# Kernel tuning notes

Hardware: AMD Instinct MI355X
Metric: run time of the kernel (lower is better)

Reference implementation:

```python
import jax, jax.numpy as jnp
import numpy as np

N = 65536      # bs * n_graphs * 32 electrodes
E = 1048576    # edges (avg degree 16)
H = 128        # first_hc (out_channels of GatedGraphConv)
IN = 5         # input node features
G = 16         # n_graphs (conv1d in-channels)
ELEC = 32
BS = 128
NC = 3


def setup_inputs() -> dict:
    key = jax.random.key(0)
    ks = jax.random.split(key, 14)
    s = 1.0 / np.sqrt(H)
    x = jax.random.normal(ks[0], (N, IN), dtype=jnp.float32)
    edge_index = jax.random.randint(ks[1], (2, E), 0, N, dtype=jnp.int32)
    edge_attr = jax.random.uniform(ks[2], (E,), dtype=jnp.float32)
    gconv_w = jax.random.normal(ks[3], (2, H, H), dtype=jnp.float32) * s
    gru_w_ih = jax.random.normal(ks[4], (3 * H, H), dtype=jnp.float32) * s
    gru_w_hh = jax.random.normal(ks[5], (3 * H, H), dtype=jnp.float32) * s
    gru_b_ih = jax.random.normal(ks[6], (3 * H,), dtype=jnp.float32) * s
    gru_b_hh = jax.random.normal(ks[7], (3 * H,), dtype=jnp.float32) * s
    conv_w = jax.random.normal(ks[8], (1, G, 3), dtype=jnp.float32) * (1.0 / np.sqrt(G * 3))
    conv_b = jax.random.normal(ks[9], (1,), dtype=jnp.float32) * 0.1
    L = (H - 3) // 2 + 1  # 63
    lin1_w = jax.random.normal(ks[10], (H, ELEC * L), dtype=jnp.float32) * (1.0 / np.sqrt(ELEC * L))
    lin1_b = jnp.zeros((H,), dtype=jnp.float32)
    lin2_w = jax.random.normal(ks[11], (NC, H), dtype=jnp.float32) * s
    lin2_b = jnp.zeros((NC,), dtype=jnp.float32)
    return {"x": x, "edge_index": edge_index, "edge_attr": edge_attr, "bs": BS,
            "gconv_w": gconv_w, "gru_w_ih": gru_w_ih, "gru_w_hh": gru_w_hh,
            "gru_b_ih": gru_b_ih, "gru_b_hh": gru_b_hh,
            "conv_w": conv_w, "conv_b": conv_b,
            "lin1_w": lin1_w, "lin1_b": lin1_b, "lin2_w": lin2_w, "lin2_b": lin2_b}


def _gated_graph_conv(x, edge_index, edge_attr, gconv_w, w_ih, w_hh, b_ih, b_hh):
    n = x.shape[0]
    # pad input features up to H (PyG GatedGraphConv behavior when in < out)
    h = jnp.concatenate([x, jnp.zeros((n, H - x.shape[1]), dtype=x.dtype)], axis=1)
    src, dst = edge_index[0], edge_index[1]
    for i in range(2):  # num_layers = 2
        m = h @ gconv_w[i]                              # [N, H]
        msg = m[src] * edge_attr[:, None]               # gather + edge weight
        agg = jax.ops.segment_sum(msg, dst, num_segments=n)  # scatter-add
        # GRUCell(agg, h)
        gi = agg @ w_ih.T + b_ih
        gh = h @ w_hh.T + b_hh
        i_r, i_z, i_n = jnp.split(gi, 3, axis=1)
        h_r, h_z, h_n = jnp.split(gh, 3, axis=1)
        r = jax.nn.sigmoid(i_r + h_r)
        z = jax.nn.sigmoid(i_z + h_z)
        nn_ = jnp.tanh(i_n + r * h_n)
        h = (1.0 - z) * nn_ + z * h
    return h


def reference(x, edge_index, edge_attr, bs, gconv_w, gru_w_ih, gru_w_hh,
              gru_b_ih, gru_b_hh, conv_w, conv_b, lin1_w, lin1_b, lin2_w, lin2_b):
    h = _gated_graph_conv(x, edge_index, edge_attr, gconv_w,
                          gru_w_ih, gru_w_hh, gru_b_ih, gru_b_hh)
    h = jax.nn.relu(h)  # dropout is identity in eval mode
    g = h.shape[0] // (bs * ELEC)
    # (bs g e) f -> (bs e) g f
    h = h.reshape(bs, g, ELEC, H).transpose(0, 2, 1, 3).reshape(bs * ELEC, g, H)
    h = jax.lax.conv_general_dilated(h, conv_w, window_strides=(2,), padding='VALID',
                                     dimension_numbers=('NCH', 'OIH', 'NCH'))
    h = h + conv_b[None, :, None]
    h = jax.nn.relu(h[:, 0, :])                 # squeeze channel -> [bs*e, L]
    h = h.reshape(bs, -1)                       # (bs e) f -> bs (e f)
    h = jax.nn.relu(h @ lin1_w.T + lin1_b)
    h = h @ lin2_w.T + lin2_b
    return jax.nn.softmax(h, axis=-1)
```

## Files before the change

kernel.cpp:

```cpp
#include <hip/hip_runtime.h>
#include <math.h>

#define NN 65536
#define NE 1048576
#define HH 128
#define ELEC 32
#define BSZ 128
#define NB 512

typedef unsigned short ushort_t;
typedef __bf16 bf16x8 __attribute__((ext_vector_type(8)));
typedef float f32x16 __attribute__((ext_vector_type(16)));

#define MFMA(A, B, C) __builtin_amdgcn_mfma_f32_32x32x16_bf16(A, B, C, 0, 0, 0)

__device__ __forceinline__ float sigm(float x) { return 1.f / (1.f + __expf(-x)); }
__device__ __forceinline__ float tanh_fast(float x) { return 2.f / (1.f + __expf(-2.f * x)) - 1.f; }

__device__ __forceinline__ float bf2f(ushort_t u) {
    union { unsigned int i; float f; } v; v.i = ((unsigned int)u) << 16; return v.f;
}
__device__ __forceinline__ ushort_t f2bf(float f) {
    union { float f; unsigned int i; } v; v.f = f;
    unsigned int r = (v.i + 0x7fffu + ((v.i >> 16) & 1u)) >> 16;
    return (ushort_t)r;
}


__global__ void k_init(const float* __restrict__ x, ushort_t* __restrict__ xh) {
    int i = blockIdx.x * 256 + threadIdx.x;
    int n = i >> 7, c = i & 127;
    float v = (c < 5) ? x[n * 5 + c] : 0.f;
    xh[(size_t)n * 256 + 128 + c] = f2bf(v);
}

__global__ __launch_bounds__(256) void k_bhist(const int* __restrict__ dst,
                                               int* __restrict__ bcnt) {
    __shared__ int h[NB];
    int t = threadIdx.x;
    h[t] = 0; h[t + 256] = 0;
    __syncthreads();
    int e0 = blockIdx.x * 4096;
    #pragma unroll
    for (int i = 0; i < 16; ++i)
        atomicAdd(&h[dst[e0 + i * 256 + t] >> 7], 1);
    __syncthreads();
    int c0 = h[t];       if (c0) atomicAdd(&bcnt[t], c0);
    int c1 = h[t + 256]; if (c1) atomicAdd(&bcnt[t + 256], c1);
}

__global__ void k_bscan(const int* __restrict__ bcnt, int* __restrict__ boffs,
                        int* __restrict__ bcur) {
    __shared__ int s[NB];
    int t = threadIdx.x;
    int v = bcnt[t];
    s[t] = v;
    __syncthreads();
    for (int d = 1; d < NB; d <<= 1) {
        int u = (t >= d) ? s[t - d] : 0;
        __syncthreads();
        s[t] += u;
        __syncthreads();
    }
    int ex = s[t] - v;
    boffs[t] = ex;
    bcur[t] = ex;
    if (t == NB - 1) boffs[NB] = s[t];
}

__global__ __launch_bounds__(256) void k_bpart(const int* __restrict__ src,
        const int* __restrict__ dst, const float* __restrict__ ea,
        int* __restrict__ bcur, uint2* __restrict__ ebkt) {
    __shared__ int lcnt[NB];
    __shared__ int base[NB];
    __shared__ int lcur[NB];
    int t = threadIdx.x;
    lcnt[t] = 0; lcnt[t + 256] = 0;
    lcur[t] = 0; lcur[t + 256] = 0;
    __syncthreads();
    int e0 = blockIdx.x * 4096;
    #pragma unroll
    for (int i = 0; i < 16; ++i)
        atomicAdd(&lcnt[dst[e0 + i * 256 + t] >> 7], 1);
    __syncthreads();
    {
        int c = lcnt[t];
        base[t] = c ? atomicAdd(&bcur[t], c) : 0;
        c = lcnt[t + 256];
        base[t + 256] = c ? atomicAdd(&bcur[t + 256], c) : 0;
    }
    __syncthreads();
    #pragma unroll
    for (int i = 0; i < 16; ++i) {
        int e = e0 + i * 256 + t;
        int d = dst[e];
        int bk = d >> 7;
        int pos = base[bk] + atomicAdd(&lcur[bk], 1);
        uint2 pk;
        pk.x = (unsigned int)src[e] | ((unsigned int)(d & 127) << 16);
        pk.y = __float_as_uint(ea[e]);
        ebkt[pos] = pk;
    }
}

__global__ __launch_bounds__(256) void k_csc(const int* __restrict__ boffs,
        const uint2* __restrict__ ebkt, uint2* __restrict__ epack,
        int* __restrict__ offs) {
    __shared__ int cnt[128];
    __shared__ int s[128];
    __shared__ int base[128];
    int b = blockIdx.x, t = threadIdx.x;
    if (t < 128) cnt[t] = 0;
    __syncthreads();
    int e0 = boffs[b], e1 = boffs[b + 1];
    for (int i = e0 + t; i < e1; i += 256)
        atomicAdd(&cnt[(ebkt[i].x >> 16) & 127], 1);
    __syncthreads();
    if (t < 128) s[t] = cnt[t];
    __syncthreads();
    for (int d = 1; d < 128; d <<= 1) {
        int v = (t < 128 && t >= d) ? s[t - d] : 0;
        __syncthreads();
        if (t < 128) s[t] += v;
        __syncthreads();
    }
    if (t < 128) {
        int bs = e0 + s[t] - cnt[t];
        base[t] = bs;
        offs[b * 128 + t] = bs;
        cnt[t] = 0;
    }
    if (b == 0 && t == 255) offs[NN] = NE;
    __syncthreads();
    for (int i = e0 + t; i < e1; i += 256) {
        uint2 e = ebkt[i];
        int dl = (e.x >> 16) & 127;
        int pos = base[dl] + atomicAdd(&cnt[dl], 1);
        epack[pos] = e;
    }
}

__global__ void k_prep(const float* __restrict__ wih, const float* __restrict__ whh,
                       const float* __restrict__ gw,
                       ushort_t* __restrict__ vp, ushort_t* __restrict__ gp) {
    int b = blockIdx.x, t = threadIdx.x;
    if (b < 512) {
        int i = b * 256 + t;
        int rho = i >> 8, k = i & 255;
        int q = rho >> 7, g = (rho >> 5) & 3, cc = rho & 31;
        int c = q * 32 + cc;
        float v;
        if (g == 0)      v = (k < 128) ? wih[c * 128 + k]          : whh[c * 128 + k - 128];
        else if (g == 1) v = (k < 128) ? wih[(128 + c) * 128 + k]  : whh[(128 + c) * 128 + k - 128];
        else if (g == 2) v = (k < 128) ? wih[(256 + c) * 128 + k]  : 0.f;
        else             v = (k < 128) ? 0.f                       : whh[(256 + c) * 128 + k - 128];
        int ks = k >> 4, lh = (k >> 3) & 1, j = k & 7, lr = cc;
        vp[(size_t)(ks * 16 + q * 4 + g) * 512 + (lh * 32 + lr) * 8 + j] = f2bf(v);
    } else {
        int i = (b - 512) * 256 + t;
        int l = i >> 14, r = i & 16383, c = r >> 7, k = r & 127;
        float v = gw[l * 16384 + k * 128 + c];
        int ct = c >> 5, lr = c & 31;
        int ks = k >> 4, lh = (k >> 3) & 1, j = k & 7;
        gp[(size_t)((l * 8 + ks) * 4 + ct) * 512 + (lh * 32 + lr) * 8 + j] = f2bf(v);
    }
}

__global__ __launch_bounds__(256, 2) void k_mgemm(const ushort_t* __restrict__ gp,
        const ushort_t* __restrict__ xh, ushort_t* __restrict__ m) {
    int t = threadIdx.x;
    int lane = t & 63, w = t >> 6;
    int lr = lane & 31, lh = lane >> 5;
    int n0 = blockIdx.x * 256 + w * 64;
    f32x16 acc[2][4];
    #pragma unroll
    for (int nt = 0; nt < 2; ++nt)
        #pragma unroll
        for (int ct = 0; ct < 4; ++ct)
            #pragma unroll
            for (int r = 0; r < 16; ++r) acc[nt][ct][r] = 0.f;
    size_t rowA0 = (size_t)(n0 + lr) * 256 + 128;
    size_t rowA1 = rowA0 + 32 * 256;
    #pragma unroll
    for (int ks = 0; ks < 8; ++ks) {
        int kg = ks * 16 + lh * 8;
        bf16x8 ah0 = *reinterpret_cast<const bf16x8*>(xh + rowA0 + kg);
        bf16x8 ah1 = *reinterpret_cast<const bf16x8*>(xh + rowA1 + kg);
        #pragma unroll
        for (int ct = 0; ct < 4; ++ct) {
            bf16x8 bh = *reinterpret_cast<const bf16x8*>(gp + (size_t)(ks * 4 + ct) * 512 + lane * 8);
            acc[0][ct] = MFMA(ah0, bh, acc[0][ct]);
            acc[1][ct] = MFMA(ah1, bh, acc[1][ct]);
        }
    }
    #pragma unroll
    for (int nt = 0; nt < 2; ++nt)
        #pragma unroll
        for (int ct = 0; ct < 4; ++ct)
            #pragma unroll
            for (int r = 0; r < 16; ++r) {
                int row = (r & 3) + 8 * (r >> 2) + 4 * lh;
                m[(size_t)(n0 + nt * 32 + row) * 128 + ct * 32 + lr] = f2bf(acc[nt][ct][r]);
            }
}

__global__ __launch_bounds__(256) void k_gather(const ushort_t* __restrict__ m,
        const int* __restrict__ offs, const uint2* __restrict__ epack,
        ushort_t* __restrict__ xh) {
    int n = blockIdx.x * 4 + (threadIdx.x >> 6);
    int lane = threadIdx.x & 63;
    int k0 = offs[n], k1 = offs[n + 1];
    float a0 = 0.f, a1 = 0.f;
    int k = k0;
    if (k < k1 && (k & 1)) {
        uint2 e = epack[k];
        float w = __uint_as_float(e.y);
        ushort2 u = *reinterpret_cast<const ushort2*>(m + (size_t)(e.x & 0xFFFFu) * HH + 2 * lane);
        a0 = fmaf(w, bf2f(u.x), a0);
        a1 = fmaf(w, bf2f(u.y), a1);
        ++k;
    }
    for (; k + 4 <= k1; k += 4) {
        uint4 e01 = *reinterpret_cast<const uint4*>(epack + k);
        uint4 e23 = *reinterpret_cast<const uint4*>(epack + k + 2);
        ushort2 u0 = *reinterpret_cast<const ushort2*>(m + (size_t)(e01.x & 0xFFFFu) * HH + 2 * lane);
        ushort2 u1 = *reinterpret_cast<const ushort2*>(m + (size_t)(e01.z & 0xFFFFu) * HH + 2 * lane);
        ushort2 u2 = *reinterpret_cast<const ushort2*>(m + (size_t)(e23.x & 0xFFFFu) * HH + 2 * lane);
        ushort2 u3 = *reinterpret_cast<const ushort2*>(m + (size_t)(e23.z & 0xFFFFu) * HH + 2 * lane);
        float w0 = __uint_as_float(e01.y), w1 = __uint_as_float(e01.w);
        float w2 = __uint_as_float(e23.y), w3 = __uint_as_float(e23.w);
        a0 = fmaf(w0, bf2f(u0.x), a0); a1 = fmaf(w0, bf2f(u0.y), a1);
        a0 = fmaf(w1, bf2f(u1.x), a0); a1 = fmaf(w1, bf2f(u1.y), a1);
        a0 = fmaf(w2, bf2f(u2.x), a0); a1 = fmaf(w2, bf2f(u2.y), a1);
        a0 = fmaf(w3, bf2f(u3.x), a0); a1 = fmaf(w3, bf2f(u3.y), a1);
    }
    if (k + 2 <= k1) {
        uint4 e01 = *reinterpret_cast<const uint4*>(epack + k);
        ushort2 u0 = *reinterpret_cast<const ushort2*>(m + (size_t)(e01.x & 0xFFFFu) * HH + 2 * lane);
        ushort2 u1 = *reinterpret_cast<const ushort2*>(m + (size_t)(e01.z & 0xFFFFu) * HH + 2 * lane);
        float w0 = __uint_as_float(e01.y), w1 = __uint_as_float(e01.w);
        a0 = fmaf(w0, bf2f(u0.x), a0); a1 = fmaf(w0, bf2f(u0.y), a1);
        a0 = fmaf(w1, bf2f(u1.x), a0); a1 = fmaf(w1, bf2f(u1.y), a1);
        k += 2;
    }
    if (k < k1) {
        uint2 e = epack[k];
        float w = __uint_as_float(e.y);
        ushort2 u = *reinterpret_cast<const ushort2*>(m + (size_t)(e.x & 0xFFFFu) * HH + 2 * lane);
        a0 = fmaf(w, bf2f(u.x), a0);
        a1 = fmaf(w, bf2f(u.y), a1);
    }
    ushort2 o; o.x = f2bf(a0); o.y = f2bf(a1);
    *reinterpret_cast<ushort2*>(xh + (size_t)n * 256 + 2 * lane) = o;
}

__global__ __launch_bounds__(256, 2) void k_gru(const ushort_t* __restrict__ vp,
        ushort_t* __restrict__ xh,
        const float* __restrict__ bih, const float* __restrict__ bhh) {
    int t = threadIdx.x;
    int lane = t & 63, q = t >> 6;
    int lr = lane & 31, lh = lane >> 5;
    int n0 = blockIdx.x * 64;
    f32x16 acc[2][4];
    #pragma unroll
    for (int nt = 0; nt < 2; ++nt)
        #pragma unroll
        for (int g = 0; g < 4; ++g)
            #pragma unroll
            for (int r = 0; r < 16; ++r) acc[nt][g][r] = 0.f;

    size_t rowA0 = (size_t)(n0 + lr) * 256;
    size_t rowA1 = rowA0 + 32 * 256;
    #pragma unroll
    for (int ks = 0; ks < 16; ++ks) {
        int kg = ks * 16 + lh * 8;
        bf16x8 ah0 = *reinterpret_cast<const bf16x8*>(xh + rowA0 + kg);
        bf16x8 ah1 = *reinterpret_cast<const bf16x8*>(xh + rowA1 + kg);
        #pragma unroll
        for (int g = 0; g < 4; ++g) {
            bf16x8 b = *reinterpret_cast<const bf16x8*>(vp + (size_t)(ks * 16 + q * 4 + g) * 512 + lane * 8);
            acc[0][g] = MFMA(ah0, b, acc[0][g]);
            acc[1][g] = MFMA(ah1, b, acc[1][g]);
        }
    }

    __syncthreads();

    int c = q * 32 + lr;
    float brz = bih[c] + bhh[c];
    float bzz = bih[128 + c] + bhh[128 + c];
    float bin = bih[256 + c];
    float bhn = bhh[256 + c];
    #pragma unroll
    for (int nt = 0; nt < 2; ++nt) {
        #pragma unroll
        for (int r = 0; r < 16; ++r) {
            int node = n0 + nt * 32 + (r & 3) + 8 * (r >> 2) + 4 * lh;
            float rg = sigm(acc[nt][0][r] + brz);
            float zg = sigm(acc[nt][1][r] + bzz);
            float nn = tanh_fast(acc[nt][2][r] + bin + rg * (acc[nt][3][r] + bhn));
            size_t idx = (size_t)node * 256 + 128 + c;
            float hold = bf2f(xh[idx]);
            float hnew = (1.f - zg) * nn + zg * hold;
            xh[idx] = f2bf(hnew);
        }
    }
}

__global__ __launch_bounds__(64) void k_conv(const ushort_t* __restrict__ xh,
        const float* __restrict__ cw, const float* __restrict__ cb,
        float* __restrict__ co) {
    __shared__ float tile[16 * 128];
    __shared__ float w[48];
    int be = blockIdx.x;
    int b = be >> 5, e = be & 31;
    int t = threadIdx.x;
    if (t < 48) w[t] = cw[t];
    #pragma unroll
    for (int i = 0; i < 8; ++i) {
        int f = t + i * 64;
        int g = f >> 5, c4 = f & 31;
        size_t idx = (size_t)(b * 512 + g * 32 + e) * 256 + 128 + c4 * 4;
        ushort4 vh4 = *reinterpret_cast<const ushort4*>(xh + idx);
        float* dst = tile + g * 128 + c4 * 4;
        dst[0] = fmaxf(bf2f(vh4.x), 0.f);
        dst[1] = fmaxf(bf2f(vh4.y), 0.f);
        dst[2] = fmaxf(bf2f(vh4.z), 0.f);
        dst[3] = fmaxf(bf2f(vh4.w), 0.f);
    }
    __syncthreads();
    if (t < 63) {
        float s = cb[0];
        #pragma unroll
        for (int g = 0; g < 16; ++g) {
            const float* p = tile + g * 128 + 2 * t;
            s = fmaf(p[0], w[g * 3 + 0], s);
            s = fmaf(p[1], w[g * 3 + 1], s);
            s = fmaf(p[2], w[g * 3 + 2], s);
        }
        co[b * 2016 + e * 63 + t] = fmaxf(s, 0.f);
    }
}

__global__ __launch_bounds__(128) void k_lin1(const float* __restrict__ co,
        const float* __restrict__ w, const float* __restrict__ bias,
        float* __restrict__ fc1) {
    __shared__ float v[2016];
    int b = blockIdx.x, t = threadIdx.x;
    for (int i = t; i < 2016; i += 128) v[i] = co[b * 2016 + i];
    __syncthreads();
    float s = bias[t];
    const float* wr = w + t * 2016;
    for (int k = 0; k < 2016; k += 4) {
        float4 wv = *reinterpret_cast<const float4*>(wr + k);
        s = fmaf(wv.x, v[k + 0], s);
        s = fmaf(wv.y, v[k + 1], s);
        s = fmaf(wv.z, v[k + 2], s);
        s = fmaf(wv.w, v[k + 3], s);
    }
    fc1[b * 128 + t] = fmaxf(s, 0.f);
}

__global__ __launch_bounds__(128) void k_lin2(const float* __restrict__ fc1,
        const float* __restrict__ w, const float* __restrict__ bias,
        float* __restrict__ out) {
    int b = threadIdx.x;
    float s0 = bias[0], s1 = bias[1], s2 = bias[2];
    const float* v = fc1 + b * 128;
    for (int k = 0; k < 128; ++k) {
        float x = v[k];
        s0 = fmaf(x, w[k], s0);
        s1 = fmaf(x, w[128 + k], s1);
        s2 = fmaf(x, w[256 + k], s2);
    }
    float mx = fmaxf(s0, fmaxf(s1, s2));
    float e0 = __expf(s0 - mx), e1 = __expf(s1 - mx), e2 = __expf(s2 - mx);
    float inv = 1.f / (e0 + e1 + e2);
    out[b * 3 + 0] = e0 * inv;
    out[b * 3 + 1] = e1 * inv;
    out[b * 3 + 2] = e2 * inv;
}

extern "C" void kernel_launch(void* const* d_in, const int* in_sizes, int n_in,
                              void* d_out, int out_size, void* d_ws, size_t ws_size,
                              hipStream_t stream) {
    const float* x   = (const float*)d_in[0];
    const int*   ei  = (const int*)d_in[1];
    const float* ea  = (const float*)d_in[2];
    const float* gw  = (const float*)d_in[4];
    const float* wih = (const float*)d_in[5];
    const float* whh = (const float*)d_in[6];
    const float* bih = (const float*)d_in[7];
    const float* bhh = (const float*)d_in[8];
    const float* cw  = (const float*)d_in[9];
    const float* cb  = (const float*)d_in[10];
    const float* l1w = (const float*)d_in[11];
    const float* l1b = (const float*)d_in[12];
    const float* l2w = (const float*)d_in[13];
    const float* l2b = (const float*)d_in[14];
    float* out = (float*)d_out;

    char* p = (char*)d_ws;
    ushort_t* xh  = (ushort_t*)p; p += (size_t)NN * 256 * 2;
    ushort_t* vp  = (ushort_t*)p; p += 512 * 256 * 2;
    ushort_t* gp  = (ushort_t*)p; p += 2 * 128 * 128 * 2;
    ushort_t* m   = (ushort_t*)p; p += (size_t)NN * HH * 2;
    uint2* ebkt   = (uint2*)p;   p += (size_t)NE * 8;
    uint2* epack  = (uint2*)p;   p += (size_t)NE * 8;
    float* co  = (float*)p; p += (size_t)BSZ * 2016 * 4;
    float* fc1 = (float*)p; p += (size_t)BSZ * HH * 4;
    int* bcnt  = (int*)p; p += NB * 4;
    int* boffs = (int*)p; p += (NB + 1) * 4;
    int* bcur  = (int*)p; p += NB * 4;
    int* offs  = (int*)p; p += (size_t)(NN + 1) * 4;

    const int* src = ei;
    const int* dst = ei + NE;

    k_prep<<<640, 256, 0, stream>>>(wih, whh, gw, vp, gp);
    hipMemsetAsync(bcnt, 0, NB * 4, stream);
    k_bhist<<<256, 256, 0, stream>>>(dst, bcnt);
    k_bscan<<<1, 512, 0, stream>>>(bcnt, boffs, bcur);
    k_bpart<<<256, 256, 0, stream>>>(src, dst, ea, bcur, ebkt);
    k_csc<<<NB, 256, 0, stream>>>(boffs, ebkt, epack, offs);
    k_init<<<(NN * 128) / 256, 256, 0, stream>>>(x, xh);

    for (int layer = 0; layer < 2; ++layer) {
        k_mgemm<<<NN / 256, 256, 0, stream>>>(gp + (size_t)layer * 16384, xh, m);
        k_gather<<<NN / 4, 256, 0, stream>>>(m, offs, epack, xh);
        k_gru<<<NN / 64, 256, 0, stream>>>(vp, xh, bih, bhh);
    }

    k_conv<<<BSZ * ELEC, 64, 0, stream>>>(xh, cw, cb, co);
    k_lin1<<<BSZ, 128, 0, stream>>>(co, l1w, l1b, fc1);
    k_lin2<<<1, 128, 0, stream>>>(fc1, l2w, l2b, out);
}
```

Before: 401.5 us.

## Fuse edge aggregation into GRU kernel via swizzled LDS staging

Merges the separate gather and GRU kernels into one kernel. Each block first aggregates messages for its 64 nodes into a bank-swizzled shared-memory tile, then runs the GRU MFMA with the aggregated half read from LDS. The hidden state buffer shrinks from a 256-wide concatenated layout to 128 wide. This removes the aggregate round trip through global memory and one launch per layer. In exchange, each wave walks 16 nodes serially during the gather phase, which lowers gather parallelism and latency hiding, and the 16KB LDS tile may affect occupancy.

```diff
diff --git a/kernel.cpp b/kernel.cpp
--- a/kernel.cpp
+++ b/kernel.cpp
@@ -27,26 +27,26 @@
 }
 
 
-__global__ void k_init(const float* __restrict__ x, ushort_t* __restrict__ xh) {
+__global__ void k_init(const float* __restrict__ x, ushort_t* __restrict__ h) {
     int i = blockIdx.x * 256 + threadIdx.x;
     int n = i >> 7, c = i & 127;
     float v = (c < 5) ? x[n * 5 + c] : 0.f;
-    xh[(size_t)n * 256 + 128 + c] = f2bf(v);
+    h[(size_t)n * 128 + c] = f2bf(v);
 }
 
 __global__ __launch_bounds__(256) void k_bhist(const int* __restrict__ dst,
                                                int* __restrict__ bcnt) {
-    __shared__ int h[NB];
-    int t = threadIdx.x;
-    h[t] = 0; h[t + 256] = 0;
+    __shared__ int hh[NB];
+    int t = threadIdx.x;
+    hh[t] = 0; hh[t + 256] = 0;
     __syncthreads();
     int e0 = blockIdx.x * 4096;
     #pragma unroll
     for (int i = 0; i < 16; ++i)
-        atomicAdd(&h[dst[e0 + i * 256 + t] >> 7], 1);
-    __syncthreads();
-    int c0 = h[t];       if (c0) atomicAdd(&bcnt[t], c0);
-    int c1 = h[t + 256]; if (c1) atomicAdd(&bcnt[t + 256], c1);
+        atomicAdd(&hh[dst[e0 + i * 256 + t] >> 7], 1);
+    __syncthreads();
+    int c0 = hh[t];       if (c0) atomicAdd(&bcnt[t], c0);
+    int c1 = hh[t + 256]; if (c1) atomicAdd(&bcnt[t + 256], c1);
 }
 
 __global__ void k_bscan(const int* __restrict__ bcnt, int* __restrict__ boffs,
@@ -167,7 +167,7 @@
 }
 
 __global__ __launch_bounds__(256, 2) void k_mgemm(const ushort_t* __restrict__ gp,
-        const ushort_t* __restrict__ xh, ushort_t* __restrict__ m) {
+        const ushort_t* __restrict__ h, ushort_t* __restrict__ m) {
     int t = threadIdx.x;
     int lane = t & 63, w = t >> 6;
     int lr = lane & 31, lh = lane >> 5;
@@ -179,13 +179,13 @@
         for (int ct = 0; ct < 4; ++ct)
             #pragma unroll
             for (int r = 0; r < 16; ++r) acc[nt][ct][r] = 0.f;
-    size_t rowA0 = (size_t)(n0 + lr) * 256 + 128;
-    size_t rowA1 = rowA0 + 32 * 256;
+    size_t rowA0 = (size_t)(n0 + lr) * 128;
+    size_t rowA1 = rowA0 + 32 * 128;
     #pragma unroll
     for (int ks = 0; ks < 8; ++ks) {
         int kg = ks * 16 + lh * 8;
-        bf16x8 ah0 = *reinterpret_cast<const bf16x8*>(xh + rowA0 + kg);
-        bf16x8 ah1 = *reinterpret_cast<const bf16x8*>(xh + rowA1 + kg);
+        bf16x8 ah0 = *reinterpret_cast<const bf16x8*>(h + rowA0 + kg);
+        bf16x8 ah1 = *reinterpret_cast<const bf16x8*>(h + rowA1 + kg);
         #pragma unroll
         for (int ct = 0; ct < 4; ++ct) {
             bf16x8 bh = *reinterpret_cast<const bf16x8*>(gp + (size_t)(ks * 4 + ct) * 512 + lane * 8);
@@ -204,63 +204,79 @@
             }
 }
 
-__global__ __launch_bounds__(256) void k_gather(const ushort_t* __restrict__ m,
+__global__ __launch_bounds__(256, 2) void k_aggru(const ushort_t* __restrict__ m,
         const int* __restrict__ offs, const uint2* __restrict__ epack,
-        ushort_t* __restrict__ xh) {
-    int n = blockIdx.x * 4 + (threadIdx.x >> 6);
-    int lane = threadIdx.x & 63;
-    int k0 = offs[n], k1 = offs[n + 1];
-    float a0 = 0.f, a1 = 0.f;
-    int k = k0;
-    if (k < k1 && (k & 1)) {
-        uint2 e = epack[k];
-        float w = __uint_as_float(e.y);
-        ushort2 u = *reinterpret_cast<const ushort2*>(m + (size_t)(e.x & 0xFFFFu) * HH + 2 * lane);
-        a0 = fmaf(w, bf2f(u.x), a0);
-        a1 = fmaf(w, bf2f(u.y), a1);
-        ++k;
-    }
-    for (; k + 4 <= k1; k += 4) {
-        uint4 e01 = *reinterpret_cast<const uint4*>(epack + k);
-        uint4 e23 = *reinterpret_cast<const uint4*>(epack + k + 2);
-        ushort2 u0 = *reinterpret_cast<const ushort2*>(m + (size_t)(e01.x & 0xFFFFu) * HH + 2 * lane);
-        ushort2 u1 = *reinterpret_cast<const ushort2*>(m + (size_t)(e01.z & 0xFFFFu) * HH + 2 * lane);
-        ushort2 u2 = *reinterpret_cast<const ushort2*>(m + (size_t)(e23.x & 0xFFFFu) * HH + 2 * lane);
-        ushort2 u3 = *reinterpret_cast<const ushort2*>(m + (size_t)(e23.z & 0xFFFFu) * HH + 2 * lane);
-        float w0 = __uint_as_float(e01.y), w1 = __uint_as_float(e01.w);
-        float w2 = __uint_as_float(e23.y), w3 = __uint_as_float(e23.w);
-        a0 = fmaf(w0, bf2f(u0.x), a0); a1 = fmaf(w0, bf2f(u0.y), a1);
-        a0 = fmaf(w1, bf2f(u1.x), a0); a1 = fmaf(w1, bf2f(u1.y), a1);
-        a0 = fmaf(w2, bf2f(u2.x), a0); a1 = fmaf(w2, bf2f(u2.y), a1);
-        a0 = fmaf(w3, bf2f(u3.x), a0); a1 = fmaf(w3, bf2f(u3.y), a1);
-    }
-    if (k + 2 <= k1) {
-        uint4 e01 = *reinterpret_cast<const uint4*>(epack + k);
-        ushort2 u0 = *reinterpret_cast<const ushort2*>(m + (size_t)(e01.x & 0xFFFFu) * HH + 2 * lane);
-        ushort2 u1 = *reinterpret_cast<const ushort2*>(m + (size_t)(e01.z & 0xFFFFu) * HH + 2 * lane);
-        float w0 = __uint_as_float(e01.y), w1 = __uint_as_float(e01.w);
-        a0 = fmaf(w0, bf2f(u0.x), a0); a1 = fmaf(w0, bf2f(u0.y), a1);
-        a0 = fmaf(w1, bf2f(u1.x), a0); a1 = fmaf(w1, bf2f(u1.y), a1);
-        k += 2;
-    }
-    if (k < k1) {
-        uint2 e = epack[k];
-        float w = __uint_as_float(e.y);
-        ushort2 u = *reinterpret_cast<const ushort2*>(m + (size_t)(e.x & 0xFFFFu) * HH + 2 * lane);
-        a0 = fmaf(w, bf2f(u.x), a0);
-        a1 = fmaf(w, bf2f(u.y), a1);
-    }
-    ushort2 o; o.x = f2bf(a0); o.y = f2bf(a1);
-    *reinterpret_cast<ushort2*>(xh + (size_t)n * 256 + 2 * lane) = o;
-}
-
-__global__ __launch_bounds__(256, 2) void k_gru(const ushort_t* __restrict__ vp,
-        ushort_t* __restrict__ xh,
+        const ushort_t* __restrict__ vp, ushort_t* __restrict__ h,
         const float* __restrict__ bih, const float* __restrict__ bhh) {
+    __shared__ ushort_t aggl[64 * 128];
     int t = threadIdx.x;
     int lane = t & 63, q = t >> 6;
+    int n0 = blockIdx.x * 64;
+
+    {
+        int chunk = lane >> 2;
+        int woff = (lane & 3) * 2;
+        for (int nl = q * 16; nl < q * 16 + 16; ++nl) {
+            int n = n0 + nl;
+            int k0 = offs[n], k1 = offs[n + 1];
+            float a0 = 0.f, a1 = 0.f;
+            int k = k0;
+            for (; k + 8 <= k1; k += 8) {
+                uint4 ea_ = *reinterpret_cast<const uint4*>(epack + k);
+                uint4 eb_ = *reinterpret_cast<const uint4*>(epack + k + 2);
+                uint4 ec_ = *reinterpret_cast<const uint4*>(epack + k + 4);
+                uint4 ed_ = *reinterpret_cast<const uint4*>(epack + k + 6);
+                ushort2 u0 = *reinterpret_cast<const ushort2*>(m + (size_t)(ea_.x & 0xFFFFu) * HH + 2 * lane);
+                ushort2 u1 = *reinterpret_cast<const ushort2*>(m + (size_t)(ea_.z & 0xFFFFu) * HH + 2 * lane);
+                ushort2 u2 = *reinterpret_cast<const ushort2*>(m + (size_t)(eb_.x & 0xFFFFu) * HH + 2 * lane);
+                ushort2 u3 = *reinterpret_cast<const ushort2*>(m + (size_t)(eb_.z & 0xFFFFu) * HH + 2 * lane);
+                ushort2 u4 = *reinterpret_cast<const ushort2*>(m + (size_t)(ec_.x & 0xFFFFu) * HH + 2 * lane);
+                ushort2 u5 = *reinterpret_cast<const ushort2*>(m + (size_t)(ec_.z & 0xFFFFu) * HH + 2 * lane);
+                ushort2 u6 = *reinterpret_cast<const ushort2*>(m + (size_t)(ed_.x & 0xFFFFu) * HH + 2 * lane);
+                ushort2 u7 = *reinterpret_cast<const ushort2*>(m + (size_t)(ed_.z & 0xFFFFu) * HH + 2 * lane);
+                float w0 = __uint_as_float(ea_.y), w1 = __uint_as_float(ea_.w);
+                float w2 = __uint_as_float(eb_.y), w3 = __uint_as_float(eb_.w);
+                float w4 = __uint_as_float(ec_.y), w5 = __uint_as_float(ec_.w);
+                float w6 = __uint_as_float(ed_.y), w7 = __uint_as_float(ed_.w);
+                a0 = fmaf(w0, bf2f(u0.x), a0); a1 = fmaf(w0, bf2f(u0.y), a1);
+                a0 = fmaf(w1, bf2f(u1.x), a0); a1 = fmaf(w1, bf2f(u1.y), a1);
+                a0 = fmaf(w2, bf2f(u2.x), a0); a1 = fmaf(w2, bf2f(u2.y), a1);
+                a0 = fmaf(w3, bf2f(u3.x), a0); a1 = fmaf(w3, bf2f(u3.y), a1);
+                a0 = fmaf(w4, bf2f(u4.x), a0); a1 = fmaf(w4, bf2f(u4.y), a1);
+                a0 = fmaf(w5, bf2f(u5.x), a0); a1 = fmaf(w5, bf2f(u5.y), a1);
+                a0 = fmaf(w6, bf2f(u6.x), a0); a1 = fmaf(w6, bf2f(u6.y), a1);
+                a0 = fmaf(w7, bf2f(u7.x), a0); a1 = fmaf(w7, bf2f(u7.y), a1);
+            }
+            if (k + 4 <= k1) {
+                uint4 ea_ = *reinterpret_cast<const uint4*>(epack + k);
+                uint4 eb_ = *reinterpret_cast<const uint4*>(epack + k + 2);
+                ushort2 u0 = *reinterpret_cast<const ushort2*>(m + (size_t)(ea_.x & 0xFFFFu) * HH + 2 * lane);
+                ushort2 u1 = *reinterpret_cast<const ushort2*>(m + (size_t)(ea_.z & 0xFFFFu) * HH + 2 * lane);
+                ushort2 u2 = *reinterpret_cast<const ushort2*>(m + (size_t)(eb_.x & 0xFFFFu) * HH + 2 * lane);
+                ushort2 u3 = *reinterpret_cast<const ushort2*>(m + (size_t)(eb_.z & 0xFFFFu) * HH + 2 * lane);
+                float w0 = __uint_as_float(ea_.y), w1 = __uint_as_float(ea_.w);
+                float w2 = __uint_as_float(eb_.y), w3 = __uint_as_float(eb_.w);
+                a0 = fmaf(w0, bf2f(u0.x), a0); a1 = fmaf(w0, bf2f(u0.y), a1);
+                a0 = fmaf(w1, bf2f(u1.x), a0); a1 = fmaf(w1, bf2f(u1.y), a1);
+                a0 = fmaf(w2, bf2f(u2.x), a0); a1 = fmaf(w2, bf2f(u2.y), a1);
+                a0 = fmaf(w3, bf2f(u3.x), a0); a1 = fmaf(w3, bf2f(u3.y), a1);
+                k += 4;
+            }
+            for (; k < k1; ++k) {
+                uint2 e = epack[k];
+                float w = __uint_as_float(e.y);
+                ushort2 u = *reinterpret_cast<const ushort2*>(m + (size_t)(e.x & 0xFFFFu) * HH + 2 * lane);
+                a0 = fmaf(w, bf2f(u.x), a0);
+                a1 = fmaf(w, bf2f(u.y), a1);
+            }
+            ushort2 o; o.x = f2bf(a0); o.y = f2bf(a1);
+            int sw = chunk ^ (nl & 15);
+            *reinterpret_cast<ushort2*>(aggl + nl * 128 + sw * 8 + woff) = o;
+        }
+    }
+    __syncthreads();
+
     int lr = lane & 31, lh = lane >> 5;
-    int n0 = blockIdx.x * 64;
     f32x16 acc[2][4];
     #pragma unroll
     for (int nt = 0; nt < 2; ++nt)
@@ -269,13 +285,20 @@
             #pragma unroll
             for (int r = 0; r < 16; ++r) acc[nt][g][r] = 0.f;
 
-    size_t rowA0 = (size_t)(n0 + lr) * 256;
-    size_t rowA1 = rowA0 + 32 * 256;
+    size_t rowH0 = (size_t)(n0 + lr) * 128;
+    size_t rowH1 = rowH0 + 32 * 128;
     #pragma unroll
     for (int ks = 0; ks < 16; ++ks) {
-        int kg = ks * 16 + lh * 8;
-        bf16x8 ah0 = *reinterpret_cast<const bf16x8*>(xh + rowA0 + kg);
-        bf16x8 ah1 = *reinterpret_cast<const bf16x8*>(xh + rowA1 + kg);
+        bf16x8 ah0, ah1;
+        if (ks < 8) {
+            int sw = ((ks * 2 + lh) ^ (lr & 15)) * 8;
+            ah0 = *reinterpret_cast<const bf16x8*>(aggl + lr * 128 + sw);
+            ah1 = *reinterpret_cast<const bf16x8*>(aggl + (32 + lr) * 128 + sw);
+        } else {
+            int kg = (ks - 8) * 16 + lh * 8;
+            ah0 = *reinterpret_cast<const bf16x8*>(h + rowH0 + kg);
+            ah1 = *reinterpret_cast<const bf16x8*>(h + rowH1 + kg);
+        }
         #pragma unroll
         for (int g = 0; g < 4; ++g) {
             bf16x8 b = *reinterpret_cast<const bf16x8*>(vp + (size_t)(ks * 16 + q * 4 + g) * 512 + lane * 8);
@@ -299,15 +322,15 @@
             float rg = sigm(acc[nt][0][r] + brz);
             float zg = sigm(acc[nt][1][r] + bzz);
             float nn = tanh_fast(acc[nt][2][r] + bin + rg * (acc[nt][3][r] + bhn));
-            size_t idx = (size_t)node * 256 + 128 + c;
-            float hold = bf2f(xh[idx]);
+            size_t idx = (size_t)node * 128 + c;
+            float hold = bf2f(h[idx]);
             float hnew = (1.f - zg) * nn + zg * hold;
-            xh[idx] = f2bf(hnew);
-        }
-    }
-}
-
-__global__ __launch_bounds__(64) void k_conv(const ushort_t* __restrict__ xh,
+            h[idx] = f2bf(hnew);
+        }
+    }
+}
+
+__global__ __launch_bounds__(64) void k_conv(const ushort_t* __restrict__ h,
         const float* __restrict__ cw, const float* __restrict__ cb,
         float* __restrict__ co) {
     __shared__ float tile[16 * 128];
@@ -320,8 +343,8 @@
     for (int i = 0; i < 8; ++i) {
         int f = t + i * 64;
         int g = f >> 5, c4 = f & 31;
-        size_t idx = (size_t)(b * 512 + g * 32 + e) * 256 + 128 + c4 * 4;
-        ushort4 vh4 = *reinterpret_cast<const ushort4*>(xh + idx);
+        size_t idx = (size_t)(b * 512 + g * 32 + e) * 128 + c4 * 4;
+        ushort4 vh4 = *reinterpret_cast<const ushort4*>(h + idx);
         float* dst = tile + g * 128 + c4 * 4;
         dst[0] = fmaxf(bf2f(vh4.x), 0.f);
         dst[1] = fmaxf(bf2f(vh4.y), 0.f);
@@ -401,7 +424,7 @@
     float* out = (float*)d_out;
 
     char* p = (char*)d_ws;
-    ushort_t* xh  = (ushort_t*)p; p += (size_t)NN * 256 * 2;
+    ushort_t* h   = (ushort_t*)p; p += (size_t)NN * 128 * 2;
     ushort_t* vp  = (ushort_t*)p; p += 512 * 256 * 2;
     ushort_t* gp  = (ushort_t*)p; p += 2 * 128 * 128 * 2;
     ushort_t* m   = (ushort_t*)p; p += (size_t)NN * HH * 2;
@@ -423,15 +446,14 @@
     k_bscan<<<1, 512, 0, stream>>>(bcnt, boffs, bcur);
     k_bpart<<<256, 256, 0, stream>>>(src, dst, ea, bcur, ebkt);
     k_csc<<<NB, 256, 0, stream>>>(boffs, ebkt, epack, offs);
-    k_init<<<(NN * 128) / 256, 256, 0, stream>>>(x, xh);
+    k_init<<<(NN * 128) / 256, 256, 0, stream>>>(x, h);
 
     for (int layer = 0; layer < 2; ++layer) {
-        k_mgemm<<<NN / 256, 256, 0, stream>>>(gp + (size_t)layer * 16384, xh, m);
-        k_gather<<<NN / 4, 256, 0, stream>>>(m, offs, epack, xh);
-        k_gru<<<NN / 64, 256, 0, stream>>>(vp, xh, bih, bhh);
-    }
-
-    k_conv<<<BSZ * ELEC, 64, 0, stream>>>(xh, cw, cb, co);
+        k_mgemm<<<NN / 256, 256, 0, stream>>>(gp + (size_t)layer * 16384, h, m);
+        k_aggru<<<NN / 64, 256, 0, stream>>>(m, offs, epack, vp, h, bih, bhh);
+    }
+
+    k_conv<<<BSZ * ELEC, 64, 0, stream>>>(h, cw, cb, co);
     k_lin1<<<BSZ, 128, 0, stream>>>(co, l1w, l1b, fc1);
     k_lin2<<<1, 128, 0, stream>>>(fc1, l2w, l2b, out);
 }
```

New measurement: 456.3 us. +13.6%, slower.
